# Kernel optimization log

Measured on AMD Instinct MI355X. Metric: run time of the kernel, lower is better.

## Reference

```python
import jax, jax.numpy as jnp
import numpy as np

MAX_SEQ_LEN = 128
ROPE_BASE = 10000.0
D_MODEL = 2048
N_HEADS = 16
D_HEAD = D_MODEL // N_HEADS
B = 64
T = 128


def _rope_caches(d_head, max_seq_len, base=ROPE_BASE):
    thetas = 1.0 / base ** (jnp.arange(0, d_head, 2, dtype=jnp.float32) / d_head)
    freqs = jnp.arange(max_seq_len, dtype=jnp.float32)[:, None] * thetas[None, :]
    return jnp.cos(freqs), jnp.sin(freqs)


def _apply_rope(x, cos, sin):
    # x: (..., T, d_head); cos/sin: (T, d_head/2)
    x_even = x[..., 0::2]
    x_odd = x[..., 1::2]
    rot_even = x_even * cos - x_odd * sin
    rot_odd = x_even * sin + x_odd * cos
    return jnp.stack([rot_even, rot_odd], axis=-1).reshape(x.shape)


def setup_inputs() -> dict:
    key = jax.random.key(0)
    kx, kq, kk, kv, ko = jax.random.split(key, 5)
    s = 1.0 / np.sqrt(D_MODEL)
    x = jax.random.normal(kx, (B, T, D_MODEL), dtype=jnp.float32)
    W_Q = jax.random.normal(kq, (D_MODEL, D_MODEL), dtype=jnp.float32) * s
    W_K = jax.random.normal(kk, (D_MODEL, D_MODEL), dtype=jnp.float32) * s
    W_V = jax.random.normal(kv, (D_MODEL, D_MODEL), dtype=jnp.float32) * s
    W_O = jax.random.normal(ko, (D_MODEL, D_MODEL), dtype=jnp.float32) * s
    mask = jnp.tril(jnp.ones((T, T), dtype=bool))[None, None]  # (1,1,T,T) causal
    return {"x": x, "W_Q": W_Q, "W_K": W_K, "W_V": W_V, "W_O": W_O, "mask": mask}


def reference(x, W_Q, W_K, W_V, W_O, mask):
    Bsz, Tlen, D = x.shape
    cos, sin = _rope_caches(D_HEAD, MAX_SEQ_LEN)
    cos, sin = cos[:Tlen], sin[:Tlen]

    def proj(W):
        # nn.Linear: x @ W.T ; reshape to (B, H, T, d_head)
        return (x @ W.T).reshape(Bsz, Tlen, N_HEADS, D_HEAD).transpose(0, 2, 1, 3)

    Q = _apply_rope(proj(W_Q), cos, sin)
    K = _apply_rope(proj(W_K), cos, sin)
    V = proj(W_V)

    scale = jnp.float32(np.sqrt(D_HEAD))
    scores = jnp.einsum("bhqd,bhkd->bhqk", Q, K) / scale
    scores = jnp.where(mask, scores, -jnp.inf)
    weights = jax.nn.softmax(scores, axis=-1)
    attn = jnp.einsum("bhqk,bhkd->bhqd", weights, V)
    attn = attn.transpose(0, 2, 1, 3).reshape(Bsz, Tlen, D)
    return attn @ W_O.T
```

## Files before the change

kernel.cpp:

```cpp
#include <hip/hip_runtime.h>
#include <hip/hip_bf16.h>
#include <math.h>

#define D_MODEL 2048
#define N_HEADS 16
#define D_HEAD  128
#define BATCH   64
#define SEQ     128
#define BT      (BATCH*SEQ)
#define LDF     6144
#define KOFF    2048
#define VOFF    4096

typedef __bf16 bf16;
typedef __attribute__((ext_vector_type(8))) __bf16 bf16x8;
typedef __attribute__((ext_vector_type(4))) float  f32x4;

__device__ __forceinline__ f32x4 mfma16(bf16x8 a, bf16x8 b, f32x4 c) {
    return __builtin_amdgcn_mfma_f32_16x16x32_bf16(a, b, c, 0, 0, 0);
}

__device__ __forceinline__ bf16x8 cvt8_f32(const float* p) {
    f32x4 lo = *(const f32x4*)p;
    f32x4 hi = *(const f32x4*)(p + 4);
    bf16x8 r;
    r[0] = (bf16)lo[0]; r[1] = (bf16)lo[1]; r[2] = (bf16)lo[2]; r[3] = (bf16)lo[3];
    r[4] = (bf16)hi[0]; r[5] = (bf16)hi[1]; r[6] = (bf16)hi[2]; r[7] = (bf16)hi[3];
    return r;
}

__device__ __forceinline__ void gl2lds16(const bf16* g, bf16* l) {
    __builtin_amdgcn_global_load_lds(
        (const __attribute__((address_space(1))) void*)g,
        (__attribute__((address_space(3))) void*)l, 16, 0, 0);
}

__device__ __forceinline__ bf16x8 rope8(bf16x8 v, int tpos, int pair0) {
    bf16x8 r;
    for (int m = 0; m < 4; ++m) {
        int i = pair0 + m;
        float theta = __expf((float)(2 * i) * (-9.210340371976184f / 128.0f));
        float ang   = (float)tpos * theta;
        float sn, cs;
        __sincosf(ang, &sn, &cs);
        float e = (float)v[2 * m], o = (float)v[2 * m + 1];
        r[2 * m]     = (bf16)(e * cs - o * sn);
        r[2 * m + 1] = (bf16)(e * sn + o * cs);
    }
    return r;
}

__global__ __launch_bounds__(256) void cvt_kernel(const float* __restrict__ src,
                                                  bf16* __restrict__ dst, int n8)
{
    int i = blockIdx.x * 256 + threadIdx.x;
    if (i < n8) *(bf16x8*)(dst + (size_t)i * 8) = cvt8_f32(src + (size_t)i * 8);
}

__global__ __launch_bounds__(256) void cvt_w3(const float* __restrict__ w0,
                                              const float* __restrict__ w1,
                                              const float* __restrict__ w2,
                                              bf16* __restrict__ dst)
{
    int i   = blockIdx.x * 256 + threadIdx.x;
    int sel = i >> 19;
    int off = i & ((1 << 19) - 1);
    const float* s = (sel == 0) ? w0 : (sel == 1) ? w1 : w2;
    *(bf16x8*)(dst + (size_t)i * 8) = cvt8_f32(s + (size_t)off * 8);
}


#define BAR() __builtin_amdgcn_s_barrier()
#define SB0() __builtin_amdgcn_sched_barrier(0)

#define READS(BSEL, KS, BK) do {                                              \
    _Pragma("unroll") for (int ii = 0; ii < 8; ++ii)                          \
        Fa[BK][ii] = *(const bf16x8*)&As[BSEL][aoff[ii] + ksw[KS]];           \
    _Pragma("unroll") for (int jj = 0; jj < 4; ++jj)                          \
        Fb[BK][jj] = *(const bf16x8*)&Bs[BSEL][bof[jj] + ksw[KS]];            \
    } while (0)

#define MQ32(BK) do {                                                         \
    __builtin_amdgcn_s_setprio(1);                                            \
    _Pragma("unroll") for (int ii = 0; ii < 8; ++ii)                          \
    _Pragma("unroll") for (int jj = 0; jj < 4; ++jj)                          \
        acc[ii][jj] = mfma16(Fa[BK][ii], Fb[BK][jj], acc[ii][jj]);            \
    __builtin_amdgcn_s_setprio(0);                                            \
    } while (0)

#define STAGE8(BSEL, tt) do {                                                 \
    const size_t _k = (size_t)(tt) * 64;                                      \
    _Pragma("unroll") for (int c = 0; c < 4; ++c) {                           \
        gl2lds16(Ag + (size_t)c * 64 * lda + _k, &As[BSEL][c*4096 + w*512]);  \
        gl2lds16(Bg + (size_t)c * 64 * ldb + _k, &Bs[BSEL][c*4096 + w*512]);  \
    } } while (0)

#define TILE(BSEL, OSEL, tt, MODE) do {                                       \
     \
    if (MODE == 0) STAGE8(OSEL, (tt) + 1);                                    \
    READS(BSEL, 1, 1);                                                        \
    SB0(); BAR();                                                             \
    asm volatile("s_waitcnt lgkmcnt(12)" ::: "memory"); SB0();                \
    MQ32(0);                                                                  \
    if (MODE == 0) asm volatile("s_waitcnt vmcnt(0)" ::: "memory");           \
    SB0(); BAR();                                                             \
            \
    if (MODE == 0) READS(OSEL, 0, 0);                                         \
    SB0(); BAR();                                                             \
    if (MODE == 0) { asm volatile("s_waitcnt lgkmcnt(12)" ::: "memory"); }    \
    else           { asm volatile("s_waitcnt lgkmcnt(0)"  ::: "memory"); }    \
    SB0();                                                                    \
    MQ32(1);                                                                  \
    SB0(); BAR();                                                             \
    } while (0)

template<typename OutT>
__global__ __launch_bounds__(512, 2) void gemm256(const bf16* __restrict__ A,
                                                  const bf16* __restrict__ B,
                                                  OutT* __restrict__ C,
                                                  int lda, int ldb, int ldc,
                                                  int K, int gx)
{
    __shared__ __align__(16) bf16 As[2][16384];
    __shared__ __align__(16) bf16 Bs[2][16384];

    const int tid  = threadIdx.x;
    const int w    = tid >> 6;
    const int l    = tid & 63;
    const int quad = l >> 4;
    const int ln   = l & 15;
    const int wm   = w >> 2;
    const int wn   = w & 3;

    const int nwg = gridDim.x;
    const int bid = blockIdx.x;
    const int swz = (bid & 7) * (nwg >> 3) + (bid >> 3);
    const int bx  = swz % gx;
    const int by  = swz / gx;
    const size_t mbase = (size_t)by * 256;
    const size_t nbase = (size_t)bx * 256;

    const int srow   = tid >> 3;
    const int schunk = (tid & 7) ^ (srow & 7);
    const bf16* Ag = A + (mbase + srow) * (size_t)lda + schunk * 8;
    const bf16* Bg = B + (nbase + srow) * (size_t)ldb + schunk * 8;

    const int xr = ln & 7;
    int aoff[8], bof[4], ksw[2];
#pragma unroll
    for (int i = 0; i < 8; ++i) aoff[i] = (wm * 128 + i * 16 + ln) * 64;
#pragma unroll
    for (int j = 0; j < 4; ++j) bof[j]  = (wn * 64  + j * 16 + ln) * 64;
#pragma unroll
    for (int kk = 0; kk < 2; ++kk) ksw[kk] = ((kk * 4 + quad) ^ xr) * 8;

    f32x4 acc[8][4];
#pragma unroll
    for (int i = 0; i < 8; ++i)
#pragma unroll
        for (int j = 0; j < 4; ++j) acc[i][j] = (f32x4){0.f, 0.f, 0.f, 0.f};

    bf16x8 Fa[2][8];
    bf16x8 Fb[2][4];

    STAGE8(0, 0);
    asm volatile("s_waitcnt vmcnt(0)" ::: "memory");
    BAR();
    READS(0, 0, 0);

    const int NT = K >> 6;
    int t = 0;
#pragma unroll 1
    for (; t < NT - 2; t += 2) {
        TILE(0, 1, t, 0);
        TILE(1, 0, t + 1, 0);
    }
    TILE(0, 1, NT - 2, 0);
    TILE(1, 0, NT - 1, 1);

#pragma unroll
    for (int i = 0; i < 8; ++i)
#pragma unroll
        for (int j = 0; j < 4; ++j)
#pragma unroll
            for (int r = 0; r < 4; ++r) {
                size_t row = mbase + wm * 128 + i * 16 + quad * 4 + r;
                size_t col = nbase + wn * 64 + j * 16 + ln;
                C[row * (size_t)ldc + col] = (OutT)acc[i][j][r];
            }
}

#undef BAR
#undef SB0
#undef READS
#undef MQ32
#undef STAGE8
#undef TILE

__global__ __launch_bounds__(256) void attn_kernel(bf16* __restrict__ buf)
{
    __shared__ __align__(16) bf16 KP_lds[128 * 136];
    __shared__ __align__(16) bf16 Vt_lds[128 * 136];

    const int bh = blockIdx.x;
    const int b  = bh >> 4;
    const int h  = bh & 15;
    const size_t baseQ = (size_t)b * SEQ * LDF + (size_t)h * D_HEAD;
    const size_t baseK = baseQ + KOFF;
    const size_t baseV = baseQ + VOFF;

    const int tid  = threadIdx.x;
    const int w    = tid >> 6;
    const int l    = tid & 63;
    const int quad = l >> 4;
    const int ln   = l & 15;

    {
        int k  = tid >> 1;
        int d0 = (tid & 1) * 64;
        const bf16* kp = buf + baseK + (size_t)k * LDF + d0;
        const bf16* vp = buf + baseV + (size_t)k * LDF + d0;
        for (int c = 0; c < 8; ++c) {
            bf16x8 kv = *(const bf16x8*)(kp + c * 8);
            *(bf16x8*)&KP_lds[k * 136 + d0 + c * 8] = rope8(kv, k, d0 / 2 + c * 4);
            bf16x8 vv = *(const bf16x8*)(vp + c * 8);
            for (int j = 0; j < 8; ++j)
                Vt_lds[(d0 + c * 8 + j) * 136 + k] = vv[j];
        }
    }
    __syncthreads();

    const float rscale = 0.08838834764831845f;
    const float NEG    = -1e30f;

    f32x4 acc2[2][8];
    for (int s = 0; s < 2; ++s)
        for (int nt = 0; nt < 8; ++nt) acc2[s][nt] = (f32x4){0.f, 0.f, 0.f, 0.f};

    for (int s = 0; s < 2; ++s) {
        const int q0 = w * 32 + s * 16;
        for (int kt = 0; kt < 4; ++kt) {
            bf16x8 qa = *(const bf16x8*)(buf + baseQ + (size_t)(q0 + ln) * LDF
                                           + kt * 32 + quad * 8);
            bf16x8 a = rope8(qa, q0 + ln, kt * 16 + quad * 4);
            for (int nt = 0; nt < 8; ++nt) {
                bf16x8 bb = *(const bf16x8*)&KP_lds[(nt * 16 + ln) * 136
                                                    + kt * 32 + quad * 8];
                acc2[s][nt] = mfma16(a, bb, acc2[s][nt]);
            }
        }

        float mx[4] = {NEG, NEG, NEG, NEG};
        for (int nt = 0; nt < 8; ++nt)
            for (int r = 0; r < 4; ++r) {
                int q = q0 + quad * 4 + r;
                int c = nt * 16 + ln;
                float v = acc2[s][nt][r] * rscale;
                v = (c <= q) ? v : NEG;
                acc2[s][nt][r] = v;
                mx[r] = fmaxf(mx[r], v);
            }
        for (int m = 1; m < 16; m <<= 1)
            for (int r = 0; r < 4; ++r)
                mx[r] = fmaxf(mx[r], __shfl_xor(mx[r], m));

        float sm[4] = {0.f, 0.f, 0.f, 0.f};
        for (int nt = 0; nt < 8; ++nt)
            for (int r = 0; r < 4; ++r) {
                float p = __expf(acc2[s][nt][r] - mx[r]);
                acc2[s][nt][r] = p;
                sm[r] += p;
            }
        for (int m = 1; m < 16; m <<= 1)
            for (int r = 0; r < 4; ++r)
                sm[r] += __shfl_xor(sm[r], m);

        for (int r = 0; r < 4; ++r) sm[r] = 1.0f / sm[r];
        for (int nt = 0; nt < 8; ++nt)
            for (int r = 0; r < 4; ++r)
                acc2[s][nt][r] *= sm[r];
    }

    __syncthreads();

    for (int s = 0; s < 2; ++s)
        for (int nt = 0; nt < 8; ++nt)
            for (int r = 0; r < 4; ++r) {
                int q = w * 32 + s * 16 + quad * 4 + r;
                int c = nt * 16 + ln;
                KP_lds[q * 136 + c] = (bf16)acc2[s][nt][r];
            }

    f32x4 o[2][8];
    for (int s = 0; s < 2; ++s)
        for (int nt = 0; nt < 8; ++nt) o[s][nt] = (f32x4){0.f, 0.f, 0.f, 0.f};

    for (int kt = 0; kt < 4; ++kt) {
        bf16x8 a0 = *(const bf16x8*)&KP_lds[(w * 32 +      ln) * 136 + kt * 32 + quad * 8];
        bf16x8 a1 = *(const bf16x8*)&KP_lds[(w * 32 + 16 + ln) * 136 + kt * 32 + quad * 8];
        for (int nt = 0; nt < 8; ++nt) {
            bf16x8 bb = *(const bf16x8*)&Vt_lds[(nt * 16 + ln) * 136 + kt * 32 + quad * 8];
            o[0][nt] = mfma16(a0, bb, o[0][nt]);
            o[1][nt] = mfma16(a1, bb, o[1][nt]);
        }
    }

    for (int s = 0; s < 2; ++s)
        for (int nt = 0; nt < 8; ++nt)
            for (int r = 0; r < 4; ++r) {
                int q = w * 32 + s * 16 + quad * 4 + r;
                int d = nt * 16 + ln;
                buf[baseQ + (size_t)q * LDF + d] = (bf16)o[s][nt][r];
            }
}

extern "C" void kernel_launch(void* const* d_in, const int* in_sizes, int n_in,
                              void* d_out, int out_size, void* d_ws, size_t ws_size,
                              hipStream_t stream)
{
    const float* x  = (const float*)d_in[0];
    const float* Wq = (const float*)d_in[1];
    const float* Wk = (const float*)d_in[2];
    const float* Wv = (const float*)d_in[3];
    const float* Wo = (const float*)d_in[4];
    float* out = (float*)d_out;

    bf16* QKV = (bf16*)d_ws;
    bf16* xb  = QKV + (size_t)BT * LDF;
    bf16* WB  = xb + (size_t)BT * D_MODEL;
    bf16* WoB = xb;

    const int n8x = BT * D_MODEL / 8;
    const int n8w = D_MODEL * D_MODEL / 8;

    cvt_kernel<<<(n8x + 255) / 256, 256, 0, stream>>>(x, xb, n8x);
    cvt_w3<<<(3 * n8w) / 256, 256, 0, stream>>>(Wq, Wk, Wv, WB);

    gemm256<bf16><<<dim3((LDF / 256) * (BT / 256)), 512, 0, stream>>>(
        xb, WB, QKV, D_MODEL, D_MODEL, LDF, D_MODEL, LDF / 256);

    cvt_kernel<<<(n8w + 255) / 256, 256, 0, stream>>>(Wo, WoB, n8w);

    attn_kernel<<<BATCH * N_HEADS, 256, 0, stream>>>(QKV);

    gemm256<float><<<dim3((D_MODEL / 256) * (BT / 256)), 512, 0, stream>>>(
        QKV, WoB, out, LDF, D_MODEL, D_MODEL, D_MODEL, D_MODEL / 256);
}
```

Baseline: 569.3 us.

## Restructure GEMM main loop into quarter-tile MFMA phases with deeper global prefetch

Splits each 64-wide K tile's MFMA work into four 4x4 quarter blocks, interleaving smaller LDS fragment reads with MFMA groups and using finer lgkmcnt waits. Global-to-LDS staging now prefetches two tiles ahead (tile t+2 into the buffer just consumed), and the first two tiles are issued in the prologue. The intent is to cut barriers per tile and hide LDS and global latency behind MFMA work, and it also shrinks the A fragment register footprint. It adds risk of subtle waitcnt or buffer-reuse hazards in the pipeline and tail.

```diff
diff --git a/kernel.cpp b/kernel.cpp
--- a/kernel.cpp
+++ b/kernel.cpp
@@ -72,19 +72,24 @@
 
 #define BAR() __builtin_amdgcn_s_barrier()
 #define SB0() __builtin_amdgcn_sched_barrier(0)
-
-#define READS(BSEL, KS, BK) do {                                              \
-    _Pragma("unroll") for (int ii = 0; ii < 8; ++ii)                          \
-        Fa[BK][ii] = *(const bf16x8*)&As[BSEL][aoff[ii] + ksw[KS]];           \
+#define LGKM(n) asm volatile("s_waitcnt lgkmcnt(" #n ")" ::: "memory")
+#define VM0()   asm volatile("s_waitcnt vmcnt(0)"  ::: "memory")
+
+#define READ_A4(BSEL, mh, ks, FA) do {                                        \
+    _Pragma("unroll") for (int ii = 0; ii < 4; ++ii)                          \
+        FA[ii] = *(const bf16x8*)&As[BSEL][aoff[(mh) * 4 + ii] + ksw[ks]];    \
+    } while (0)
+
+#define READ_B4(BSEL, ks, FB) do {                                            \
     _Pragma("unroll") for (int jj = 0; jj < 4; ++jj)                          \
-        Fb[BK][jj] = *(const bf16x8*)&Bs[BSEL][bof[jj] + ksw[KS]];            \
+        FB[jj] = *(const bf16x8*)&Bs[BSEL][bof[jj] + ksw[ks]];                \
     } while (0)
 
-#define MQ32(BK) do {                                                         \
+#define MQ16(mh, FA, FB) do {                                                 \
     __builtin_amdgcn_s_setprio(1);                                            \
-    _Pragma("unroll") for (int ii = 0; ii < 8; ++ii)                          \
+    _Pragma("unroll") for (int ii = 0; ii < 4; ++ii)                          \
     _Pragma("unroll") for (int jj = 0; jj < 4; ++jj)                          \
-        acc[ii][jj] = mfma16(Fa[BK][ii], Fb[BK][jj], acc[ii][jj]);            \
+        acc[(mh) * 4 + ii][jj] = mfma16(FA[ii], FB[jj], acc[(mh) * 4 + ii][jj]); \
     __builtin_amdgcn_s_setprio(0);                                            \
     } while (0)
 
@@ -96,22 +101,31 @@
     } } while (0)
 
 #define TILE(BSEL, OSEL, tt, MODE) do {                                       \
-     \
-    if (MODE == 0) STAGE8(OSEL, (tt) + 1);                                    \
-    READS(BSEL, 1, 1);                                                        \
-    SB0(); BAR();                                                             \
-    asm volatile("s_waitcnt lgkmcnt(12)" ::: "memory"); SB0();                \
-    MQ32(0);                                                                  \
-    if (MODE == 0) asm volatile("s_waitcnt vmcnt(0)" ::: "memory");           \
-    SB0(); BAR();                                                             \
-            \
-    if (MODE == 0) READS(OSEL, 0, 0);                                         \
-    SB0(); BAR();                                                             \
-    if (MODE == 0) { asm volatile("s_waitcnt lgkmcnt(12)" ::: "memory"); }    \
-    else           { asm volatile("s_waitcnt lgkmcnt(0)"  ::: "memory"); }    \
-    SB0();                                                                    \
-    MQ32(1);                                                                  \
-    SB0(); BAR();                                                             \
+                                                                      \
+    READ_A4(BSEL, 1, 0, Fa[1]); SB0(); READ_B4(BSEL, 1, Fb[1]);               \
+    LGKM(8); SB0();                                                           \
+    MQ16(0, Fa[0], Fb[0]);                                                    \
+    SB0();                                                                    \
+                                                                      \
+    READ_A4(BSEL, 1, 1, Fa[0]);                                               \
+    LGKM(8); SB0();                                                           \
+    MQ16(1, Fa[1], Fb[0]);                                                    \
+    SB0();                                                                    \
+                                                                      \
+    VM0(); BAR(); SB0();                                                      \
+    READ_A4(BSEL, 0, 1, Fa[1]); SB0();                                        \
+    if (MODE < 2) { READ_B4(OSEL, 0, Fb[0]); LGKM(8); } else { LGKM(4); }     \
+    SB0();                                                                    \
+    MQ16(1, Fa[0], Fb[1]);                                                    \
+    SB0();                                                                    \
+                                                                      \
+    if (MODE < 2) { LGKM(4); } else { LGKM(0); }                              \
+    BAR(); SB0();                                                             \
+    if (MODE == 0) STAGE8(BSEL, (tt) + 2);                                    \
+    if (MODE < 2) READ_A4(OSEL, 0, 0, Fa[0]);                                 \
+    SB0();                                                                    \
+    MQ16(0, Fa[1], Fb[1]);                                                    \
+    SB0();                                                                    \
     } while (0)
 
 template<typename OutT>
@@ -160,13 +174,15 @@
 #pragma unroll
         for (int j = 0; j < 4; ++j) acc[i][j] = (f32x4){0.f, 0.f, 0.f, 0.f};
 
-    bf16x8 Fa[2][8];
+    bf16x8 Fa[2][4];
     bf16x8 Fb[2][4];
 
     STAGE8(0, 0);
-    asm volatile("s_waitcnt vmcnt(0)" ::: "memory");
-    BAR();
-    READS(0, 0, 0);
+    VM0();
+    BAR(); SB0();
+    STAGE8(1, 1);
+    READ_B4(0, 0, Fb[0]); SB0();
+    READ_A4(0, 0, 0, Fa[0]); SB0();
 
     const int NT = K >> 6;
     int t = 0;
@@ -175,8 +191,8 @@
         TILE(0, 1, t, 0);
         TILE(1, 0, t + 1, 0);
     }
-    TILE(0, 1, NT - 2, 0);
-    TILE(1, 0, NT - 1, 1);
+    TILE(0, 1, NT - 2, 1);
+    TILE(1, 0, NT - 1, 2);
 
 #pragma unroll
     for (int i = 0; i < 8; ++i)
@@ -192,8 +208,11 @@
 
 #undef BAR
 #undef SB0
-#undef READS
-#undef MQ32
+#undef LGKM
+#undef VM0
+#undef READ_A4
+#undef READ_B4
+#undef MQ16
 #undef STAGE8
 #undef TILE
 
```

Result: faster. 540.0 us (-5.1%).
